# Kernel optimization log

Hardware: AMD Instinct MI355X
Metric: run time of the kernel (lower is better)

Reference implementation:

```python
import jax, jax.numpy as jnp
import numpy as np

TOP_K = 2


def setup_inputs() -> dict:
    key = jax.random.key(0)
    k0, k1, k2, k3, k4 = jax.random.split(key, 5)
    B, S, D, E, F = 4, 2048, 1024, 8, 512
    return {
        "hidden_states": jax.random.normal(k0, (B, S, D), dtype=jnp.float32),
        "router_weight": jax.random.normal(k1, (E, D), dtype=jnp.float32) * 0.02,
        "w_gate": jax.random.normal(k2, (E, D, F), dtype=jnp.float32) * 0.02,
        "w_up": jax.random.normal(k3, (E, D, F), dtype=jnp.float32) * 0.02,
        "w_down": jax.random.normal(k4, (E, F, D), dtype=jnp.float32) * 0.02,
    }


def reference(hidden_states, router_weight, w_gate, w_up, w_down):
    B, S, D = hidden_states.shape
    E = router_weight.shape[0]
    x = hidden_states.reshape(-1, D)          # [T, D] token-flattened
    T = x.shape[0]

    # --- TopKRouter: softmax over experts, top-k, renormalize selected probs ---
    logits = x @ router_weight.T              # [T, E]
    probs = jax.nn.softmax(logits, axis=-1)
    top_p, top_i = jax.lax.top_k(probs, TOP_K)            # [T, k]
    top_p = top_p / jnp.sum(top_p, axis=-1, keepdims=True)  # renormalize=True

    # combine weights: scatter selected probabilities into [T, E]
    combine = jnp.zeros((T, E), x.dtype).at[jnp.arange(T)[:, None], top_i].add(top_p)

    # --- Grouped SwiGLU experts (dropless: zero combine weight => zero contribution) ---
    g = jnp.einsum('td,edf->tef', x, w_gate)  # [T, E, F]
    u = jnp.einsum('td,edf->tef', x, w_up)    # [T, E, F]
    h = jax.nn.silu(g) * u                    # SwiGLU activation
    # down-proj + weighted combine fused
    out = jnp.einsum('tef,efd,te->td', h, w_down, combine)  # [T, D]
    return out.reshape(B, S, D)
```

## Files before the change

### kernel.cpp

```cpp
#include <hip/hip_runtime.h>
#include <hip/hip_bf16.h>


typedef __attribute__((ext_vector_type(4))) float  f32x4;
typedef __attribute__((ext_vector_type(8))) unsigned short us8;
typedef __attribute__((ext_vector_type(4))) unsigned short us4;
typedef __bf16 bf16_t;
typedef __attribute__((ext_vector_type(8))) bf16_t bf16x8;

#define TTOK 8192
#define DDIM 1024
#define EEXP 8
#define FDIM 512

__device__ __forceinline__ unsigned short f2bf(float f) {
  unsigned int u = __float_as_uint(f);
  u = (u + 0x7FFFu + ((u >> 16) & 1u)) >> 16;
  return (unsigned short)u;
}

__device__ __forceinline__ float bf2f(unsigned short u) {
  return __uint_as_float((unsigned int)u << 16);
}

__device__ __forceinline__ void gload16(const void* g, void* l) {
  __builtin_amdgcn_global_load_lds(
      (const __attribute__((address_space(1))) void*)g,
      (__attribute__((address_space(3))) void*)l, 16, 0, 0);
}

__global__ __launch_bounds__(256) void k_tcvt(const float* __restrict__ src,
                                              unsigned short* __restrict__ dst,
                                              int M, int N) {
  __shared__ float tile[32][33];
  int e  = blockIdx.z;
  int m0 = blockIdx.y * 32, n0 = blockIdx.x * 32;
  const float* s = src + (size_t)e * M * N;
  unsigned short* d = dst + (size_t)e * M * N;
  int r  = threadIdx.x >> 3;
  int c4 = (threadIdx.x & 7) * 4;
  f32x4 v = *(const f32x4*)(s + (size_t)(m0 + r) * N + n0 + c4);
  tile[r][c4+0] = v[0]; tile[r][c4+1] = v[1];
  tile[r][c4+2] = v[2]; tile[r][c4+3] = v[3];
  __syncthreads();
  us4 o;
  o[0] = f2bf(tile[c4+0][r]); o[1] = f2bf(tile[c4+1][r]);
  o[2] = f2bf(tile[c4+2][r]); o[3] = f2bf(tile[c4+3][r]);
  *(us4*)(d + (size_t)(n0 + r) * M + m0 + c4) = o;
}

__global__ __launch_bounds__(256) void k_router(const float* __restrict__ x,
                                                const float* __restrict__ rw,
                                                unsigned short* __restrict__ xb,
                                                int* __restrict__ topki,
                                                float* __restrict__ topkw) {
  __shared__ float wlds[8 * 1024];
  int tid = threadIdx.x;
  #pragma unroll
  for (int i = 0; i < 8; ++i)
    ((f32x4*)wlds)[tid + i * 256] = ((const f32x4*)rw)[tid + i * 256];
  __syncthreads();

  int wv = tid >> 6, lane = tid & 63;
  int t = blockIdx.x * 4 + wv;
  const f32x4* xr = (const f32x4*)(x + (size_t)t * DDIM);
  f32x4 xv[4];
  #pragma unroll
  for (int j = 0; j < 4; ++j) xv[j] = xr[j * 64 + lane];
  #pragma unroll
  for (int j = 0; j < 4; ++j) {
    us4 o;
    o[0] = f2bf(xv[j][0]); o[1] = f2bf(xv[j][1]);
    o[2] = f2bf(xv[j][2]); o[3] = f2bf(xv[j][3]);
    *(us4*)(xb + (size_t)t * DDIM + (j * 64 + lane) * 4) = o;
  }
  double xd[16];
  #pragma unroll
  for (int j = 0; j < 4; ++j) {
    xd[j*4+0] = xv[j][0]; xd[j*4+1] = xv[j][1];
    xd[j*4+2] = xv[j][2]; xd[j*4+3] = xv[j][3];
  }
  float pf[8];
  #pragma unroll
  for (int e = 0; e < 8; ++e) {
    double acc = 0.0;
    #pragma unroll
    for (int j = 0; j < 4; ++j) {
      f32x4 wv4 = ((const f32x4*)(wlds + e * 1024))[j * 64 + lane];
      acc = fma((double)wv4[0], xd[j*4+0], acc);
      acc = fma((double)wv4[1], xd[j*4+1], acc);
      acc = fma((double)wv4[2], xd[j*4+2], acc);
      acc = fma((double)wv4[3], xd[j*4+3], acc);
    }
    pf[e] = (float)acc;
  }
  #pragma unroll
  for (int e = 0; e < 8; ++e) {
    #pragma unroll
    for (int off = 32; off >= 1; off >>= 1)
      pf[e] += __shfl_xor(pf[e], off, 64);
  }
  if (lane == 0) {
    int i1 = 0;
    #pragma unroll
    for (int e2 = 1; e2 < 8; ++e2) if (pf[e2] > pf[i1]) i1 = e2;
    int i2 = (i1 == 0) ? 1 : 0;
    #pragma unroll
    for (int e2 = 0; e2 < 8; ++e2) if (e2 != i1 && pf[e2] > pf[i2]) i2 = e2;
    float d21 = pf[i2] - pf[i1];
    float e1  = __expf(d21);
    float s   = 1.f + e1;
    topki[2*t]   = i1;       topki[2*t+1] = i2;
    topkw[2*t]   = 1.f / s;  topkw[2*t+1] = e1 / s;
  }
}

__global__ __launch_bounds__(256) void k_count(const int* __restrict__ topki,
                                               int* __restrict__ ctrs) {
  __shared__ int h[8];
  if (threadIdx.x < 8) h[threadIdx.x] = 0;
  __syncthreads();
  int i = blockIdx.x * 256 + threadIdx.x;
  atomicAdd(&h[topki[i]], 1);
  __syncthreads();
  if (threadIdx.x < 8) atomicAdd(&ctrs[threadIdx.x], h[threadIdx.x]);
}

__global__ void k_scan(int* __restrict__ ctrs) {
  if (threadIdx.x == 0 && blockIdx.x == 0) {
    ctrs[8] = 0;
    #pragma unroll
    for (int e = 0; e < 8; ++e) ctrs[9 + e] = ctrs[8 + e] + ctrs[e];
    #pragma unroll
    for (int e = 0; e < 8; ++e) ctrs[17 + e] = 0;
  }
}

__global__ __launch_bounds__(256) void k_scatter(const int* __restrict__ topki,
                                                 const float* __restrict__ topkw,
                                                 int* __restrict__ ctrs,
                                                 int* __restrict__ at,
                                                 float* __restrict__ aw,
                                                 int* __restrict__ pos) {
  __shared__ int lc[8], base[8];
  int tid = threadIdx.x;
  if (tid < 8) lc[tid] = 0;
  __syncthreads();
  int t = blockIdx.x * 256 + tid;
  int e0 = topki[2*t], e1 = topki[2*t+1];
  int r0 = atomicAdd(&lc[e0], 1);
  int r1 = atomicAdd(&lc[e1], 1);
  __syncthreads();
  if (tid < 8) base[tid] = atomicAdd(&ctrs[17 + tid], lc[tid]);
  __syncthreads();
  int a0 = ctrs[8 + e0] + base[e0] + r0;
  int a1 = ctrs[8 + e1] + base[e1] + r1;
  at[a0] = t; aw[a0] = topkw[2*t];
  at[a1] = t; aw[a1] = topkw[2*t+1];
  pos[2*t] = a0; pos[2*t+1] = a1;
}

__global__ __launch_bounds__(512, 2) void k_gateup(
    const unsigned short* __restrict__ xb,
    const unsigned short* __restrict__ wgt,
    const unsigned short* __restrict__ wut,
    const int* __restrict__ at,
    const int* __restrict__ ctrs,
    unsigned short* __restrict__ h) {
  int e    = blockIdx.z;
  int seg0 = ctrs[8 + e];
  int cnt  = ctrs[9 + e] - seg0;
  int row0 = blockIdx.y * 256;
  if (row0 >= cnt) return;
  int f0 = blockIdx.x * 128;

  __shared__ unsigned short lA [2][256 * 64];
  __shared__ unsigned short lBg[2][128 * 64];
  __shared__ unsigned short lBu[2][128 * 64];
  __shared__ int s_tok[256];

  int tid = threadIdx.x;
  if (tid < 256) {
    int rg = row0 + tid;
    s_tok[tid] = at[seg0 + ((rg < cnt) ? rg : 0)];
  }
  __syncthreads();

  const unsigned short* aSrc[4];
  size_t bOff[2];
  #pragma unroll
  for (int i = 0; i < 4; ++i) {
    int row = i * 64 + (tid >> 3);
    int su  = (tid & 7) ^ (row & 7);
    aSrc[i] = xb + (size_t)s_tok[row] * DDIM + su * 8;
  }
  #pragma unroll
  for (int j = 0; j < 2; ++j) {
    int row = j * 64 + (tid >> 3);
    int su  = (tid & 7) ^ (row & 7);
    bOff[j] = (size_t)row * DDIM + su * 8;
  }
  const unsigned short* bgBase = wgt + ((size_t)e * FDIM + f0) * DDIM;
  const unsigned short* buBase = wut + ((size_t)e * FDIM + f0) * DDIM;

  int w = tid >> 6, lane = tid & 63;
  int wr = (w >> 1) * 64, wc = (w & 1) * 64;

  f32x4 zero = {0.f, 0.f, 0.f, 0.f};
  f32x4 accg[4][4], accu[4][4];
  #pragma unroll
  for (int mt = 0; mt < 4; ++mt)
    #pragma unroll
    for (int nt = 0; nt < 4; ++nt) { accg[mt][nt] = zero; accu[mt][nt] = zero; }

  #pragma unroll
  for (int i = 0; i < 4; ++i) gload16(aSrc[i], &lA[0][(i * 512 + tid) * 8]);
  #pragma unroll
  for (int j = 0; j < 2; ++j) {
    gload16(bgBase + bOff[j], &lBg[0][(j * 512 + tid) * 8]);
    gload16(buBase + bOff[j], &lBu[0][(j * 512 + tid) * 8]);
  }
  __syncthreads();

  int cur = 0;
  for (int ks = 0; ks < DDIM / 64; ++ks) {
    if (ks + 1 < DDIM / 64) {
      int k1 = (ks + 1) * 64;
      int nx = cur ^ 1;
      #pragma unroll
      for (int i = 0; i < 4; ++i) gload16(aSrc[i] + k1, &lA[nx][(i * 512 + tid) * 8]);
      #pragma unroll
      for (int j = 0; j < 2; ++j) {
        gload16(bgBase + bOff[j] + k1, &lBg[nx][(j * 512 + tid) * 8]);
        gload16(buBase + bOff[j] + k1, &lBu[nx][(j * 512 + tid) * 8]);
      }
    }
    #pragma unroll
    for (int kk = 0; kk < 2; ++kk) {
      bf16x8 af[4];
      #pragma unroll
      for (int mt = 0; mt < 4; ++mt) {
        int ar = wr + mt * 16 + (lane & 15);
        int au = (kk * 4 + (lane >> 4)) ^ (ar & 7);
        af[mt] = *(const bf16x8*)&lA[cur][(ar * 8 + au) * 8];
      }
      #pragma unroll
      for (int nt = 0; nt < 4; ++nt) {
        int br = wc + nt * 16 + (lane & 15);
        int bu = (kk * 4 + (lane >> 4)) ^ (br & 7);
        bf16x8 bg = *(const bf16x8*)&lBg[cur][(br * 8 + bu) * 8];
        bf16x8 bv = *(const bf16x8*)&lBu[cur][(br * 8 + bu) * 8];
        #pragma unroll
        for (int mt = 0; mt < 4; ++mt) {
          accg[mt][nt] = __builtin_amdgcn_mfma_f32_16x16x32_bf16(af[mt], bg, accg[mt][nt], 0, 0, 0);
          accu[mt][nt] = __builtin_amdgcn_mfma_f32_16x16x32_bf16(af[mt], bv, accu[mt][nt], 0, 0, 0);
        }
      }
    }
    __syncthreads();
    cur ^= 1;
  }
  #pragma unroll
  for (int mt = 0; mt < 4; ++mt) {
    #pragma unroll
    for (int nt = 0; nt < 4; ++nt) {
      #pragma unroll
      for (int j = 0; j < 4; ++j) {
        int rl = wr + mt * 16 + (lane >> 4) * 4 + j;
        if (row0 + rl < cnt) {
          float g = accg[mt][nt][j], u = accu[mt][nt][j];
          float hv = g * (1.f / (1.f + __expf(-g))) * u;
          h[(size_t)(seg0 + row0 + rl) * FDIM + f0 + wc + nt * 16 + (lane & 15)] = f2bf(hv);
        }
      }
    }
  }
}

__global__ __launch_bounds__(512, 2) void k_down(
    const unsigned short* __restrict__ h,
    const unsigned short* __restrict__ wdt,
    const float* __restrict__ aw,
    const int* __restrict__ ctrs,
    unsigned short* __restrict__ y2) {
  int e    = blockIdx.z;
  int seg0 = ctrs[8 + e];
  int cnt  = ctrs[9 + e] - seg0;
  int row0 = blockIdx.y * 256;
  if (row0 >= cnt) return;
  int d0 = blockIdx.x * 256;

  __shared__ unsigned short lA[2][256 * 64];
  __shared__ unsigned short lB[2][256 * 64];
  __shared__ float s_w[256];

  int tid = threadIdx.x;
  if (tid < 256) {
    int rg = row0 + tid;
    s_w[tid] = aw[seg0 + ((rg < cnt) ? rg : 0)];
  }
  __syncthreads();

  const unsigned short* aSrc[4];
  size_t bOff[4];
  #pragma unroll
  for (int i = 0; i < 4; ++i) {
    int row = i * 64 + (tid >> 3);
    int su  = (tid & 7) ^ (row & 7);
    int rr  = (row0 + row < cnt) ? row0 + row : 0;
    aSrc[i] = h + (size_t)(seg0 + rr) * FDIM + su * 8;
    bOff[i] = (size_t)row * FDIM + su * 8;
  }
  const unsigned short* bBase = wdt + ((size_t)e * DDIM + d0) * FDIM;

  int w = tid >> 6, lane = tid & 63;
  int wr = (w >> 1) * 64, wc = (w & 1) * 128;

  f32x4 zero = {0.f, 0.f, 0.f, 0.f};
  f32x4 acc[4][8];
  #pragma unroll
  for (int mt = 0; mt < 4; ++mt)
    #pragma unroll
    for (int nt = 0; nt < 8; ++nt) acc[mt][nt] = zero;

  #pragma unroll
  for (int i = 0; i < 4; ++i) {
    gload16(aSrc[i],         &lA[0][(i * 512 + tid) * 8]);
    gload16(bBase + bOff[i], &lB[0][(i * 512 + tid) * 8]);
  }
  __syncthreads();

  int cur = 0;
  for (int ks = 0; ks < FDIM / 64; ++ks) {
    if (ks + 1 < FDIM / 64) {
      int k1 = (ks + 1) * 64;
      int nx = cur ^ 1;
      #pragma unroll
      for (int i = 0; i < 4; ++i) {
        gload16(aSrc[i] + k1,         &lA[nx][(i * 512 + tid) * 8]);
        gload16(bBase + bOff[i] + k1, &lB[nx][(i * 512 + tid) * 8]);
      }
    }
    #pragma unroll
    for (int kk = 0; kk < 2; ++kk) {
      bf16x8 af[4];
      #pragma unroll
      for (int mt = 0; mt < 4; ++mt) {
        int ar = wr + mt * 16 + (lane & 15);
        int au = (kk * 4 + (lane >> 4)) ^ (ar & 7);
        af[mt] = *(const bf16x8*)&lA[cur][(ar * 8 + au) * 8];
      }
      #pragma unroll
      for (int nt = 0; nt < 8; ++nt) {
        int br = wc + nt * 16 + (lane & 15);
        int bu = (kk * 4 + (lane >> 4)) ^ (br & 7);
        bf16x8 bf = *(const bf16x8*)&lB[cur][(br * 8 + bu) * 8];
        #pragma unroll
        for (int mt = 0; mt < 4; ++mt)
          acc[mt][nt] = __builtin_amdgcn_mfma_f32_16x16x32_bf16(af[mt], bf, acc[mt][nt], 0, 0, 0);
      }
    }
    __syncthreads();
    cur ^= 1;
  }
  #pragma unroll
  for (int mt = 0; mt < 4; ++mt) {
    #pragma unroll
    for (int nt = 0; nt < 8; ++nt) {
      #pragma unroll
      for (int j = 0; j < 4; ++j) {
        int rl = wr + mt * 16 + (lane >> 4) * 4 + j;
        if (row0 + rl < cnt) {
          float v = acc[mt][nt][j] * s_w[rl];
          y2[(size_t)(seg0 + row0 + rl) * DDIM + d0 + wc + nt * 16 + (lane & 15)] = f2bf(v);
        }
      }
    }
  }
}

__global__ __launch_bounds__(256) void k_combine(const unsigned short* __restrict__ y2,
                                                 const int* __restrict__ pos,
                                                 float* __restrict__ out) {
  int idx = blockIdx.x * 256 + threadIdx.x;
  int t = idx >> 7;
  int c = idx & 127;
  int a0 = pos[2*t], a1 = pos[2*t+1];
  us8 v0 = *((const us8*)(y2 + (size_t)a0 * DDIM) + c);
  us8 v1 = *((const us8*)(y2 + (size_t)a1 * DDIM) + c);
  f32x4 o0, o1;
  #pragma unroll
  for (int m = 0; m < 4; ++m) o0[m] = bf2f(v0[m]) + bf2f(v1[m]);
  #pragma unroll
  for (int m = 0; m < 4; ++m) o1[m] = bf2f(v0[4+m]) + bf2f(v1[4+m]);
  f32x4* dst = (f32x4*)(out + (size_t)t * DDIM + c * 8);
  dst[0] = o0; dst[1] = o1;
}

extern "C" void kernel_launch(void* const* d_in, const int* in_sizes, int n_in,
                              void* d_out, int out_size, void* d_ws, size_t ws_size,
                              hipStream_t stream) {
  (void)in_sizes; (void)n_in; (void)ws_size; (void)out_size;
  const float* x  = (const float*)d_in[0];
  const float* rw = (const float*)d_in[1];
  const float* wg = (const float*)d_in[2];
  const float* wu = (const float*)d_in[3];
  const float* wd = (const float*)d_in[4];
  float* out = (float*)d_out;

  char* ws = (char*)d_ws;
  unsigned short* xb  = (unsigned short*)(ws + 0);
  unsigned short* wgt = (unsigned short*)(ws + 16777216);
  unsigned short* wut = (unsigned short*)(ws + 25165824);
  unsigned short* y2  = (unsigned short*)(ws + 0);
  unsigned short* wdt = (unsigned short*)(ws + 33554432);
  unsigned short* hbuf= (unsigned short*)(ws + 41943040);
  float* topkw = (float*)(ws + 58720256);
  int*   topki = (int*)  (ws + 58785792);
  int*   at    = (int*)  (ws + 58851328);
  float* aw    = (float*)(ws + 58916864);
  int*   ctrs  = (int*)  (ws + 58982400);
  int*   pos   = (int*)  (ws + 58982656);

  hipMemsetAsync(ctrs, 0, 256, stream);

  k_router<<<2048, 256, 0, stream>>>(x, rw, xb, topki, topkw);
  k_tcvt <<<dim3(16, 32, 8), 256, 0, stream>>>(wg, wgt, 1024, 512);
  k_tcvt <<<dim3(16, 32, 8), 256, 0, stream>>>(wu, wut, 1024, 512);
  k_tcvt <<<dim3(32, 16, 8), 256, 0, stream>>>(wd, wdt, 512, 1024);
  k_count <<<64, 256, 0, stream>>>(topki, ctrs);
  k_scan  <<<1, 64, 0, stream>>>(ctrs);
  k_scatter<<<32, 256, 0, stream>>>(topki, topkw, ctrs, at, aw, pos);
  k_gateup<<<dim3(4, 64, 8), 512, 0, stream>>>(xb, wgt, wut, at, ctrs, hbuf);
  k_down  <<<dim3(4, 64, 8), 512, 0, stream>>>(hbuf, wdt, aw, ctrs, y2);
  k_combine<<<4096, 256, 0, stream>>>(y2, pos, out);
}
```

Before: 272.3 us.

## Overlap prefetch with MFMA via manual waitcnt, swizzle block order, merge transpose launches

The gate/up and down GEMM loops replace __syncthreads with explicit vmcnt waits. The next stage's global-to-LDS loads can then stay in flight while the current stage is computed, and the loop ends with lgkmcnt plus a barrier. Both GEMMs switch to a 1D grid whose block order is swizzled across the 8 experts, meant to spread work across XCDs and improve L2 locality. The gate and up weight transposes are merged into a single launch. The hand-placed waitcnt counts and barriers risk races if the count of outstanding loads does not match what is assumed.

```diff
diff --git a/kernel.cpp b/kernel.cpp
--- a/kernel.cpp
+++ b/kernel.cpp
@@ -13,6 +13,10 @@
 #define EEXP 8
 #define FDIM 512
 
+#define LGKM0() asm volatile("s_waitcnt lgkmcnt(0)" ::: "memory")
+#define SBAR()  __builtin_amdgcn_s_barrier()
+#define SCHEDB() __builtin_amdgcn_sched_barrier(0)
+
 __device__ __forceinline__ unsigned short f2bf(float f) {
   unsigned int u = __float_as_uint(f);
   u = (u + 0x7FFFu + ((u >> 16) & 1u)) >> 16;
@@ -29,11 +33,16 @@
       (__attribute__((address_space(3))) void*)l, 16, 0, 0);
 }
 
-__global__ __launch_bounds__(256) void k_tcvt(const float* __restrict__ src,
-                                              unsigned short* __restrict__ dst,
-                                              int M, int N) {
+__global__ __launch_bounds__(256) void k_tcvt2(const float* __restrict__ s0,
+                                               const float* __restrict__ s1,
+                                               unsigned short* __restrict__ d0,
+                                               unsigned short* __restrict__ d1,
+                                               int M, int N) {
   __shared__ float tile[32][33];
-  int e  = blockIdx.z;
+  int zz = blockIdx.z;
+  const float* src = (zz < 8) ? s0 : s1;
+  unsigned short* dst = (zz < 8) ? d0 : d1;
+  int e  = zz & 7;
   int m0 = blockIdx.y * 32, n0 = blockIdx.x * 32;
   const float* s = src + (size_t)e * M * N;
   unsigned short* d = dst + (size_t)e * M * N;
@@ -167,12 +176,16 @@
     const int* __restrict__ at,
     const int* __restrict__ ctrs,
     unsigned short* __restrict__ h) {
-  int e    = blockIdx.z;
+  int bid = blockIdx.x;
+  int swz = (bid & 7) * 256 + (bid >> 3);
+  int e   = swz >> 8;
+  int yt  = (swz & 255) >> 2;
+  int ft  = swz & 3;
   int seg0 = ctrs[8 + e];
   int cnt  = ctrs[9 + e] - seg0;
-  int row0 = blockIdx.y * 256;
+  int row0 = yt * 256;
   if (row0 >= cnt) return;
-  int f0 = blockIdx.x * 128;
+  int f0 = ft * 128;
 
   __shared__ unsigned short lA [2][256 * 64];
   __shared__ unsigned short lBg[2][128 * 64];
@@ -213,28 +226,26 @@
     #pragma unroll
     for (int nt = 0; nt < 4; ++nt) { accg[mt][nt] = zero; accu[mt][nt] = zero; }
 
-  #pragma unroll
-  for (int i = 0; i < 4; ++i) gload16(aSrc[i], &lA[0][(i * 512 + tid) * 8]);
-  #pragma unroll
-  for (int j = 0; j < 2; ++j) {
-    gload16(bgBase + bOff[j], &lBg[0][(j * 512 + tid) * 8]);
-    gload16(buBase + bOff[j], &lBu[0][(j * 512 + tid) * 8]);
-  }
-  __syncthreads();
-
+#define GU_STAGE(B, K0) do {                                              \
+    _Pragma("unroll")                                                     \
+    for (int i = 0; i < 4; ++i) gload16(aSrc[i] + (K0), &lA[B][(i * 512 + tid) * 8]); \
+    _Pragma("unroll")                                                     \
+    for (int j = 0; j < 2; ++j) {                                         \
+      gload16(bgBase + bOff[j] + (K0), &lBg[B][(j * 512 + tid) * 8]);     \
+      gload16(buBase + bOff[j] + (K0), &lBu[B][(j * 512 + tid) * 8]);     \
+    }                                                                     \
+  } while (0)
+
+  GU_STAGE(0, 0);
   int cur = 0;
   for (int ks = 0; ks < DDIM / 64; ++ks) {
     if (ks + 1 < DDIM / 64) {
-      int k1 = (ks + 1) * 64;
-      int nx = cur ^ 1;
-      #pragma unroll
-      for (int i = 0; i < 4; ++i) gload16(aSrc[i] + k1, &lA[nx][(i * 512 + tid) * 8]);
-      #pragma unroll
-      for (int j = 0; j < 2; ++j) {
-        gload16(bgBase + bOff[j] + k1, &lBg[nx][(j * 512 + tid) * 8]);
-        gload16(buBase + bOff[j] + k1, &lBu[nx][(j * 512 + tid) * 8]);
-      }
-    }
+      GU_STAGE(cur ^ 1, (ks + 1) * 64);
+      asm volatile("s_waitcnt vmcnt(8)" ::: "memory");
+    } else {
+      asm volatile("s_waitcnt vmcnt(0)" ::: "memory");
+    }
+    SBAR(); SCHEDB();
     #pragma unroll
     for (int kk = 0; kk < 2; ++kk) {
       bf16x8 af[4];
@@ -257,9 +268,11 @@
         }
       }
     }
-    __syncthreads();
+    LGKM0(); SCHEDB();
+    SBAR();
     cur ^= 1;
   }
+#undef GU_STAGE
   #pragma unroll
   for (int mt = 0; mt < 4; ++mt) {
     #pragma unroll
@@ -283,12 +296,16 @@
     const float* __restrict__ aw,
     const int* __restrict__ ctrs,
     unsigned short* __restrict__ y2) {
-  int e    = blockIdx.z;
+  int bid = blockIdx.x;
+  int swz = (bid & 7) * 256 + (bid >> 3);
+  int e   = swz >> 8;
+  int yt  = (swz & 255) >> 2;
+  int dt  = swz & 3;
   int seg0 = ctrs[8 + e];
   int cnt  = ctrs[9 + e] - seg0;
-  int row0 = blockIdx.y * 256;
+  int row0 = yt * 256;
   if (row0 >= cnt) return;
-  int d0 = blockIdx.x * 256;
+  int d0 = dt * 256;
 
   __shared__ unsigned short lA[2][256 * 64];
   __shared__ unsigned short lB[2][256 * 64];
@@ -323,24 +340,24 @@
     #pragma unroll
     for (int nt = 0; nt < 8; ++nt) acc[mt][nt] = zero;
 
-  #pragma unroll
-  for (int i = 0; i < 4; ++i) {
-    gload16(aSrc[i],         &lA[0][(i * 512 + tid) * 8]);
-    gload16(bBase + bOff[i], &lB[0][(i * 512 + tid) * 8]);
-  }
-  __syncthreads();
-
+#define DN_STAGE(B, K0) do {                                              \
+    _Pragma("unroll")                                                     \
+    for (int i = 0; i < 4; ++i) {                                         \
+      gload16(aSrc[i] + (K0),         &lA[B][(i * 512 + tid) * 8]);       \
+      gload16(bBase + bOff[i] + (K0), &lB[B][(i * 512 + tid) * 8]);       \
+    }                                                                     \
+  } while (0)
+
+  DN_STAGE(0, 0);
   int cur = 0;
   for (int ks = 0; ks < FDIM / 64; ++ks) {
     if (ks + 1 < FDIM / 64) {
-      int k1 = (ks + 1) * 64;
-      int nx = cur ^ 1;
-      #pragma unroll
-      for (int i = 0; i < 4; ++i) {
-        gload16(aSrc[i] + k1,         &lA[nx][(i * 512 + tid) * 8]);
-        gload16(bBase + bOff[i] + k1, &lB[nx][(i * 512 + tid) * 8]);
-      }
-    }
+      DN_STAGE(cur ^ 1, (ks + 1) * 64);
+      asm volatile("s_waitcnt vmcnt(8)" ::: "memory");
+    } else {
+      asm volatile("s_waitcnt vmcnt(0)" ::: "memory");
+    }
+    SBAR(); SCHEDB();
     #pragma unroll
     for (int kk = 0; kk < 2; ++kk) {
       bf16x8 af[4];
@@ -360,9 +377,11 @@
           acc[mt][nt] = __builtin_amdgcn_mfma_f32_16x16x32_bf16(af[mt], bf, acc[mt][nt], 0, 0, 0);
       }
     }
-    __syncthreads();
+    LGKM0(); SCHEDB();
+    SBAR();
     cur ^= 1;
   }
+#undef DN_STAGE
   #pragma unroll
   for (int mt = 0; mt < 4; ++mt) {
     #pragma unroll
@@ -425,13 +444,12 @@
   hipMemsetAsync(ctrs, 0, 256, stream);
 
   k_router<<<2048, 256, 0, stream>>>(x, rw, xb, topki, topkw);
-  k_tcvt <<<dim3(16, 32, 8), 256, 0, stream>>>(wg, wgt, 1024, 512);
-  k_tcvt <<<dim3(16, 32, 8), 256, 0, stream>>>(wu, wut, 1024, 512);
-  k_tcvt <<<dim3(32, 16, 8), 256, 0, stream>>>(wd, wdt, 512, 1024);
+  k_tcvt2<<<dim3(16, 32, 16), 256, 0, stream>>>(wg, wu, wgt, wut, 1024, 512);
+  k_tcvt2<<<dim3(32, 16, 8), 256, 0, stream>>>(wd, wd, wdt, wdt, 512, 1024);
   k_count <<<64, 256, 0, stream>>>(topki, ctrs);
   k_scan  <<<1, 64, 0, stream>>>(ctrs);
   k_scatter<<<32, 256, 0, stream>>>(topki, topkw, ctrs, at, aw, pos);
-  k_gateup<<<dim3(4, 64, 8), 512, 0, stream>>>(xb, wgt, wut, at, ctrs, hbuf);
-  k_down  <<<dim3(4, 64, 8), 512, 0, stream>>>(hbuf, wdt, aw, ctrs, y2);
+  k_gateup<<<2048, 512, 0, stream>>>(xb, wgt, wut, at, ctrs, hbuf);
+  k_down  <<<2048, 512, 0, stream>>>(hbuf, wdt, aw, ctrs, y2);
   k_combine<<<4096, 256, 0, stream>>>(y2, pos, out);
 }
```

Result: faster. 264.8 us (-2.7%).
